# Optimization experiments

Hardware: AMD Instinct MI355X
Metric: run time of the kernel (lower is better)

Reference implementation:

```python
import jax, jax.numpy as jnp
import numpy as np
import math

DROPOUT_P = 0.3

def setup_inputs() -> dict:
    key = jax.random.key(0)
    ks = jax.random.split(key, 8)
    B, S, D, H = 16, 2048, 1024, 128
    x = jax.random.normal(ks[0], (B, S, D), dtype=jnp.float32)
    attention_mask = jax.random.randint(ks[1], (B, S), 0, 2, dtype=jnp.int32)
    qw = 0.02 * jax.random.normal(ks[2], (H, D), dtype=jnp.float32)
    kw = 0.02 * jax.random.normal(ks[3], (H, D), dtype=jnp.float32)
    vw = 0.02 * jax.random.normal(ks[4], (H, D), dtype=jnp.float32)
    qb = jnp.zeros((H,), jnp.float32)
    kb = jnp.zeros((H,), jnp.float32)
    vb = jnp.zeros((H,), jnp.float32)
    return {"x": x, "attention_mask": attention_mask, "qw": qw, "qb": qb,
            "kw": kw, "kb": kb, "vw": vw, "vb": vb}

def reference(x, attention_mask, qw, qb, kw, kb, vw, vb):
    B, S, _ = x.shape
    H = qw.shape[0]
    # torch Linear: x @ W.T + b
    Q = jnp.einsum('bsd,hd->bsh', x, qw) + qb
    K = jnp.einsum('bsd,hd->bsh', x, kw) + kb
    V = jnp.einsum('bsd,hd->bsh', x, vw) + vb
    scores = jnp.einsum('bqh,bkh->bqk', Q, K) / math.sqrt(H)
    mask = attention_mask[:, None, :]  # [B,1,S] broadcast over queries
    scores = jnp.where(mask == 0, -jnp.inf, scores)
    probs = jax.nn.softmax(scores, axis=-1)
    # training-mode dropout with fixed key (deterministic reference)
    keep = jax.random.bernoulli(jax.random.key(42), 1.0 - DROPOUT_P, probs.shape)
    probs = jnp.where(keep, probs / (1.0 - DROPOUT_P), 0.0)
    out = jnp.einsum('bqk,bkh->bqh', probs, V)
    return out
```

## Files before the change

### kernel.cpp

```cpp
#include <hip/hip_runtime.h>
#include <stdint.h>

#define PRNG_VARIANT 2
#define USE_COMPACTION 1
#define USE_ATTN_MFMA 1

#define B_ 16
#define S_ 2048
#define D_ 1024
#define H_ 128
#define SCALE_ 0.08838834764831845f
#define KEEPP_ 0.7f

typedef __attribute__((ext_vector_type(8))) short bf16x8_t;
typedef __attribute__((ext_vector_type(4))) float f32x4_t;

__device__ __forceinline__ void threefry2x32(uint32_t x0, uint32_t x1,
                                             uint32_t& o0, uint32_t& o1) {
  const uint32_t ks0 = 0u, ks1 = 42u, ks2 = 0x1BD11BF0u;
  x0 += ks0; x1 += ks1;
#define TF_R(r) { x0 += x1; x1 = (x1 << (r)) | (x1 >> (32 - (r))); x1 ^= x0; }
  TF_R(13) TF_R(15) TF_R(26) TF_R(6)
  x0 += ks1; x1 += ks2 + 1u;
  TF_R(17) TF_R(29) TF_R(16) TF_R(24)
  x0 += ks2; x1 += ks0 + 2u;
  TF_R(13) TF_R(15) TF_R(26) TF_R(6)
  x0 += ks0; x1 += ks1 + 3u;
  TF_R(17) TF_R(29) TF_R(16) TF_R(24)
  x0 += ks1; x1 += ks2 + 4u;
  TF_R(13) TF_R(15) TF_R(26) TF_R(6)
  x0 += ks2; x1 += ks0 + 5u;
#undef TF_R
  o0 = x0; o1 = x1;
}

__device__ __forceinline__ bool keep_rand(uint32_t n) {
  uint32_t o0, o1, bits;
#if PRNG_VARIANT == 2
  threefry2x32(0u, n, o0, o1);
  bits = o0 ^ o1;
#elif PRNG_VARIANT == 1
  threefry2x32(0u, n, o0, o1);
  bits = o1;
#else
  if (n < (1u << 25)) { threefry2x32(n, n + (1u << 25), o0, o1); bits = o0; }
  else                { threefry2x32(n - (1u << 25), n, o0, o1); bits = o1; }
#endif
  float u = __uint_as_float((bits >> 9) | 0x3F800000u) - 1.0f;
  return u < KEEPP_;
}

__device__ __forceinline__ uint16_t bf16_rne(float f) {
  uint32_t u = __float_as_uint(f);
  return (uint16_t)((u + 0x7FFFu + ((u >> 16) & 1u)) >> 16);
}

__device__ __forceinline__ bf16x8_t ldf(const ushort* base, int off0, int off1) {
  union { uint2 d[2]; bf16x8_t v; } u;
  u.d[0] = *(const uint2*)(base + off0);
  u.d[1] = *(const uint2*)(base + off1);
  return u.v;
}

__global__ __launch_bounds__(64) void mask_scan(
    const int* __restrict__ amask,
    int* __restrict__ kidx, int* __restrict__ ncomp) {
  const int b = blockIdx.x;
  const int lane = threadIdx.x;
  const int* m = amask + b * S_;
  int* outp = kidx + b * S_;
  int base = 0;
  for (int c = 0; c < S_; c += 64) {
    const int mv = m[c + lane];
    const unsigned long long bal = __ballot(mv != 0);
    const int off = __popcll(bal & ((1ull << lane) - 1ull));
    if (mv != 0) outp[base + off] = c + lane;
    base += (int)__popcll(bal);
  }
  if (lane == 0) ncomp[b] = base;
  for (int i = base + lane; i < S_; i += 64) outp[i] = 0;
}

__device__ __forceinline__ bf16x8_t ld_frag(const ushort T[128][36], int row, int g) {
  union { uint2 d[2]; bf16x8_t v; } u;
  u.d[0] = *(const uint2*)&T[row][g << 2];
  u.d[1] = *(const uint2*)&T[row][16 + (g << 2)];
  return u.v;
}

__global__ __launch_bounds__(256) void qkv_mfma(
    const float* __restrict__ x,
    const float* __restrict__ qw, const float* __restrict__ qb,
    const float* __restrict__ kw, const float* __restrict__ kb,
    const float* __restrict__ vw, const float* __restrict__ vb,
    float* __restrict__ qkv) {
  __shared__ ushort Xh[128][36], Xl[128][36], Wh[128][36], Wl[128][36];

  const int tid = threadIdx.x;
  const int m0  = blockIdx.x * 128;
  const int by  = blockIdx.y;
  const float* wsrc = (by == 0) ? qw : (by == 1) ? kw : vw;
  const float* bias = (by == 0) ? qb : (by == 1) ? kb : vb;

  const int wid = tid >> 6, lane = tid & 63;
  const int wy = wid >> 1, wx = wid & 1;
  const int lm = lane & 15, g = lane >> 4;

  const int srow = tid >> 3;
  const int sc4  = (tid & 7) << 2;

  f32x4_t acc[4][4];
#pragma unroll
  for (int i = 0; i < 4; ++i)
#pragma unroll
    for (int j = 0; j < 4; ++j) acc[i][j] = (f32x4_t){0.f, 0.f, 0.f, 0.f};

  for (int k0 = 0; k0 < D_; k0 += 32) {
    __syncthreads();
#pragma unroll
    for (int i = 0; i < 4; ++i) {
      const int row = srow + (i << 5);
      {
        float4 v = *(const float4*)(x + (size_t)(m0 + row) * D_ + k0 + sc4);
        uint16_t h0 = bf16_rne(v.x), h1 = bf16_rne(v.y),
                 h2 = bf16_rne(v.z), h3 = bf16_rne(v.w);
        float r0 = v.x - __uint_as_float((uint32_t)h0 << 16);
        float r1 = v.y - __uint_as_float((uint32_t)h1 << 16);
        float r2 = v.z - __uint_as_float((uint32_t)h2 << 16);
        float r3 = v.w - __uint_as_float((uint32_t)h3 << 16);
        *(uint2*)&Xh[row][sc4] = make_uint2((uint32_t)h0 | ((uint32_t)h1 << 16),
                                            (uint32_t)h2 | ((uint32_t)h3 << 16));
        *(uint2*)&Xl[row][sc4] = make_uint2(
            (uint32_t)bf16_rne(r0) | ((uint32_t)bf16_rne(r1) << 16),
            (uint32_t)bf16_rne(r2) | ((uint32_t)bf16_rne(r3) << 16));
      }
      {
        float4 v = *(const float4*)(wsrc + (size_t)row * D_ + k0 + sc4);
        uint16_t h0 = bf16_rne(v.x), h1 = bf16_rne(v.y),
                 h2 = bf16_rne(v.z), h3 = bf16_rne(v.w);
        float r0 = v.x - __uint_as_float((uint32_t)h0 << 16);
        float r1 = v.y - __uint_as_float((uint32_t)h1 << 16);
        float r2 = v.z - __uint_as_float((uint32_t)h2 << 16);
        float r3 = v.w - __uint_as_float((uint32_t)h3 << 16);
        *(uint2*)&Wh[row][sc4] = make_uint2((uint32_t)h0 | ((uint32_t)h1 << 16),
                                            (uint32_t)h2 | ((uint32_t)h3 << 16));
        *(uint2*)&Wl[row][sc4] = make_uint2(
            (uint32_t)bf16_rne(r0) | ((uint32_t)bf16_rne(r1) << 16),
            (uint32_t)bf16_rne(r2) | ((uint32_t)bf16_rne(r3) << 16));
      }
    }
    __syncthreads();

    bf16x8_t Ah[4], Al[4], Bh[4], Bl[4];
#pragma unroll
    for (int mi = 0; mi < 4; ++mi) {
      const int r = (wy << 6) + (mi << 4) + lm;
      Ah[mi] = ld_frag(Xh, r, g);
      Al[mi] = ld_frag(Xl, r, g);
    }
#pragma unroll
    for (int ni = 0; ni < 4; ++ni) {
      const int r = (wx << 6) + (ni << 4) + lm;
      Bh[ni] = ld_frag(Wh, r, g);
      Bl[ni] = ld_frag(Wl, r, g);
    }
#pragma unroll
    for (int mi = 0; mi < 4; ++mi)
#pragma unroll
      for (int ni = 0; ni < 4; ++ni) {
        acc[mi][ni] = __builtin_amdgcn_mfma_f32_16x16x32_bf16(
            Ah[mi], Bh[ni], acc[mi][ni], 0, 0, 0);
        acc[mi][ni] = __builtin_amdgcn_mfma_f32_16x16x32_bf16(
            Ah[mi], Bl[ni], acc[mi][ni], 0, 0, 0);
        acc[mi][ni] = __builtin_amdgcn_mfma_f32_16x16x32_bf16(
            Al[mi], Bh[ni], acc[mi][ni], 0, 0, 0);
      }
  }

#pragma unroll
  for (int mi = 0; mi < 4; ++mi) {
    const int row = m0 + (wy << 6) + (mi << 4) + (g << 2);
#pragma unroll
    for (int ni = 0; ni < 4; ++ni) {
      const int nl = (wx << 6) + (ni << 4) + lm;
      const float bv = bias[nl];
#pragma unroll
      for (int r = 0; r < 4; ++r)
        qkv[(size_t)(row + r) * 384 + (by << 7) + nl] = acc[mi][ni][r] + bv;
    }
  }
}

__global__ __launch_bounds__(128) void attn_mfma(
    const float* __restrict__ qkv,
    const int* __restrict__ kidx,
    const int* __restrict__ ncomp,
    float* __restrict__ out) {
  __shared__ ushort KhS[32][132], KlS[32][132];
  __shared__ ushort Vt[128][36];
  __shared__ int kidx_s[32];

  const int b   = blockIdx.y;
  const int q0  = blockIdx.x * 32;
  const int tid = threadIdx.x;
  const int wid = tid >> 6, lane = tid & 63;
  const int g = lane >> 4, lm = lane & 15;
  const int nc = ncomp[b];
  const int* kidx_b = kidx + b * S_;
  const int qrow = q0 + wid * 16 + lm;

  bf16x8_t Qh[4], Ql[4];
  {
    const float* qptr = qkv + (size_t)(b * S_ + qrow) * 384;
#pragma unroll
    for (int c = 0; c < 4; ++c) {
      float4 ea = *(const float4*)(qptr + 32 * c + 4 * g);
      float4 eb = *(const float4*)(qptr + 32 * c + 16 + 4 * g);
      float f[8] = {ea.x, ea.y, ea.z, ea.w, eb.x, eb.y, eb.z, eb.w};
      union { ushort u[8]; bf16x8_t v; } hh, ll;
#pragma unroll
      for (int e = 0; e < 8; ++e) {
        float s = f[e] * SCALE_;
        ushort h = bf16_rne(s);
        hh.u[e] = h;
        ll.u[e] = bf16_rne(s - __uint_as_float((uint32_t)h << 16));
      }
      Qh[c] = hh.v; Ql[c] = ll.v;
    }
  }

  f32x4_t acc[8];
#pragma unroll
  for (int t = 0; t < 8; ++t) acc[t] = (f32x4_t){0.f, 0.f, 0.f, 0.f};
  float m_run = -INFINITY, l_run = 0.f;
  const uint32_t nq = (uint32_t)(b * S_ + qrow) << 11;

  for (int kt = 0; kt < nc; kt += 32) {
    __syncthreads();
    if (tid < 32) kidx_s[tid] = kidx_b[kt + tid];
#pragma unroll
    for (int i = 0; i < 8; ++i) {
      int flat = i * 128 + tid;
      int key = flat >> 5, c4 = (flat & 31) << 2;
      int krow = kidx_b[kt + key];
      float4 v = *(const float4*)(qkv + ((size_t)(b * S_ + krow) * 384 + 128) + c4);
      uint16_t h0 = bf16_rne(v.x), h1 = bf16_rne(v.y),
               h2 = bf16_rne(v.z), h3 = bf16_rne(v.w);
      float r0 = v.x - __uint_as_float((uint32_t)h0 << 16);
      float r1 = v.y - __uint_as_float((uint32_t)h1 << 16);
      float r2 = v.z - __uint_as_float((uint32_t)h2 << 16);
      float r3 = v.w - __uint_as_float((uint32_t)h3 << 16);
      *(uint2*)&KhS[key][c4] = make_uint2((uint32_t)h0 | ((uint32_t)h1 << 16),
                                          (uint32_t)h2 | ((uint32_t)h3 << 16));
      *(uint2*)&KlS[key][c4] = make_uint2(
          (uint32_t)bf16_rne(r0) | ((uint32_t)bf16_rne(r1) << 16),
          (uint32_t)bf16_rne(r2) | ((uint32_t)bf16_rne(r3) << 16));
    }
#pragma unroll
    for (int i = 0; i < 8; ++i) {
      int flat = i * 128 + tid;
      int key = flat >> 5, c4 = (flat & 31) << 2;
      int krow = kidx_b[kt + key];
      float4 v = *(const float4*)(qkv + ((size_t)(b * S_ + krow) * 384 + 256) + c4);
      Vt[c4 + 0][key] = bf16_rne(v.x);
      Vt[c4 + 1][key] = bf16_rne(v.y);
      Vt[c4 + 2][key] = bf16_rne(v.z);
      Vt[c4 + 3][key] = bf16_rne(v.w);
    }
    __syncthreads();

    f32x4_t s0 = (f32x4_t){0.f, 0.f, 0.f, 0.f};
    f32x4_t s1 = (f32x4_t){0.f, 0.f, 0.f, 0.f};
#pragma unroll
    for (int c = 0; c < 4; ++c) {
      const int o0 = 32 * c + 4 * g, o1 = 32 * c + 16 + 4 * g;
      bf16x8_t a0h = ldf(&KhS[lm][0], o0, o1);
      bf16x8_t a0l = ldf(&KlS[lm][0], o0, o1);
      bf16x8_t a1h = ldf(&KhS[lm + 16][0], o0, o1);
      bf16x8_t a1l = ldf(&KlS[lm + 16][0], o0, o1);
      s0 = __builtin_amdgcn_mfma_f32_16x16x32_bf16(a0h, Qh[c], s0, 0, 0, 0);
      s0 = __builtin_amdgcn_mfma_f32_16x16x32_bf16(a0l, Qh[c], s0, 0, 0, 0);
      s0 = __builtin_amdgcn_mfma_f32_16x16x32_bf16(a0h, Ql[c], s0, 0, 0, 0);
      s1 = __builtin_amdgcn_mfma_f32_16x16x32_bf16(a1h, Qh[c], s1, 0, 0, 0);
      s1 = __builtin_amdgcn_mfma_f32_16x16x32_bf16(a1l, Qh[c], s1, 0, 0, 0);
      s1 = __builtin_amdgcn_mfma_f32_16x16x32_bf16(a1h, Ql[c], s1, 0, 0, 0);
    }

    float sv0[4], sv1[4];
#pragma unroll
    for (int r = 0; r < 4; ++r) {
      sv0[r] = (kt + 4 * g + r      < nc) ? s0[r] : -INFINITY;
      sv1[r] = (kt + 16 + 4 * g + r < nc) ? s1[r] : -INFINITY;
    }
    float tm = fmaxf(fmaxf(fmaxf(sv0[0], sv0[1]), fmaxf(sv0[2], sv0[3])),
                     fmaxf(fmaxf(sv1[0], sv1[1]), fmaxf(sv1[2], sv1[3])));
    tm = fmaxf(tm, __shfl_xor(tm, 16));
    tm = fmaxf(tm, __shfl_xor(tm, 32));
    float mn = fmaxf(m_run, tm);

    float p0[4], p1[4], ps = 0.f;
#pragma unroll
    for (int r = 0; r < 4; ++r) {
      p0[r] = (sv0[r] == -INFINITY) ? 0.f : __expf(sv0[r] - mn);
      p1[r] = (sv1[r] == -INFINITY) ? 0.f : __expf(sv1[r] - mn);
      ps += p0[r] + p1[r];
    }
    ps += __shfl_xor(ps, 16);
    ps += __shfl_xor(ps, 32);

    float rf = (m_run == mn) ? 1.f : __expf(m_run - mn);
    l_run = l_run * rf + ps;
    m_run = mn;

    float fr0 = __shfl(rf, 4 * g + 0);
    float fr1 = __shfl(rf, 4 * g + 1);
    float fr2 = __shfl(rf, 4 * g + 2);
    float fr3 = __shfl(rf, 4 * g + 3);
#pragma unroll
    for (int t = 0; t < 8; ++t) {
      acc[t][0] *= fr0; acc[t][1] *= fr1; acc[t][2] *= fr2; acc[t][3] *= fr3;
    }

    union { ushort u[8]; bf16x8_t v; } pk;
#pragma unroll
    for (int r = 0; r < 4; ++r) {
      float dv0 = keep_rand(nq + (uint32_t)kidx_s[4 * g + r])      ? p0[r] : 0.f;
      float dv1 = keep_rand(nq + (uint32_t)kidx_s[16 + 4 * g + r]) ? p1[r] : 0.f;
      pk.u[r]     = bf16_rne(dv0);
      pk.u[4 + r] = bf16_rne(dv1);
    }

#pragma unroll
    for (int ht = 0; ht < 8; ++ht) {
      bf16x8_t vf = ldf(&Vt[ht * 16 + lm][0], 4 * g, 16 + 4 * g);
      acc[ht] = __builtin_amdgcn_mfma_f32_16x16x32_bf16(pk.v, vf, acc[ht], 0, 0, 0);
    }
  }

  float iv[4];
#pragma unroll
  for (int r = 0; r < 4; ++r) {
    float lq = __shfl(l_run, 4 * g + r);
    iv[r] = 1.0f / (lq * KEEPP_);
  }
#pragma unroll
  for (int ht = 0; ht < 8; ++ht) {
#pragma unroll
    for (int r = 0; r < 4; ++r) {
      const int q = q0 + wid * 16 + 4 * g + r;
      out[(size_t)(b * S_ + q) * H_ + ht * 16 + lm] = acc[ht][r] * iv[r];
    }
  }
}

#if !USE_ATTN_MFMA
__global__ __launch_bounds__(256) void attn_fwd(
    const float* __restrict__ qkv,
    const int* __restrict__ kidx,
    const int* __restrict__ ncomp,
    float* __restrict__ out) {
  __shared__ float Qs[32][132];
  __shared__ float Ks[32][132];

  const int b   = blockIdx.y;
  const int q0  = blockIdx.x * 32;
  const int tid = threadIdx.x;
  const int ty = tid >> 4, tx = tid & 15;
  const int nc = ncomp[b];
  const int* kidx_b = kidx + b * S_;

  const float* qbase = qkv + (size_t)(b * S_ + q0) * 384;
#pragma unroll
  for (int rep = 0; rep < 4; ++rep) {
    int idx = rep * 256 + tid;
    int r = idx >> 5, c4 = (idx & 31) << 2;
    float4 v = *(const float4*)(qbase + (size_t)r * 384 + c4);
    v.x *= SCALE_; v.y *= SCALE_; v.z *= SCALE_; v.w *= SCALE_;
    *(float4*)&Qs[r][c4] = v;
  }

  const int qr = ty * 2;
  const int hx = tx * 8;

  float acc0[8], acc1[8];
#pragma unroll
  for (int h = 0; h < 8; ++h) { acc0[h] = 0.f; acc1[h] = 0.f; }
  float m0v = -INFINITY, m1v = -INFINITY, l0 = 0.f, l1 = 0.f;

  const uint32_t nq0 = (uint32_t)(b * S_ + q0 + qr) << 11;
  const uint32_t nq1 = nq0 + (1u << 11);

  for (int kt = 0; kt < nc; kt += 32) {
    __syncthreads();
#pragma unroll
    for (int rep = 0; rep < 4; ++rep) {
      int idx = rep * 256 + tid;
      int r = idx >> 5, c4 = (idx & 31) << 2;
      int krow = kidx_b[kt + r];
      *(float4*)&Ks[r][c4] =
          *(const float4*)(qkv + ((size_t)(b * S_ + krow) * 384 + 128) + c4);
    }
    const int j0 = kt + tx, j1 = j0 + 16;
    const int kr0 = kidx_b[j0];
    const int kr1 = kidx_b[j1];
    const bool kill0 = (j0 >= nc), kill1 = (j1 >= nc);
    __syncthreads();

    float s00 = 0.f, s01 = 0.f, s10 = 0.f, s11 = 0.f;
#pragma unroll 8
    for (int d = 0; d < 128; d += 4) {
      float4 qv0 = *(const float4*)&Qs[qr][d];
      float4 qv1 = *(const float4*)&Qs[qr + 1][d];
      float4 kv0 = *(const float4*)&Ks[tx][d];
      float4 kv1 = *(const float4*)&Ks[tx + 16][d];
      s00 += qv0.x * kv0.x + qv0.y * kv0.y + qv0.z * kv0.z + qv0.w * kv0.w;
      s01 += qv0.x * kv1.x + qv0.y * kv1.y + qv0.z * kv1.z + qv0.w * kv1.w;
      s10 += qv1.x * kv0.x + qv1.y * kv0.y + qv1.z * kv0.z + qv1.w * kv0.w;
      s11 += qv1.x * kv1.x + qv1.y * kv1.y + qv1.z * kv1.z + qv1.w * kv1.w;
    }
    if (kill0) { s00 = -INFINITY; s10 = -INFINITY; }
    if (kill1) { s01 = -INFINITY; s11 = -INFINITY; }

    float tm0 = fmaxf(s00, s01);
    float tm1 = fmaxf(s10, s11);
#pragma unroll
    for (int o = 1; o < 16; o <<= 1) {
      tm0 = fmaxf(tm0, __shfl_xor(tm0, o, 16));
      tm1 = fmaxf(tm1, __shfl_xor(tm1, o, 16));
    }
    float mn0 = fmaxf(m0v, tm0);
    float mn1 = fmaxf(m1v, tm1);

    float p00 = (s00 == -INFINITY) ? 0.f : __expf(s00 - mn0);
    float p01 = (s01 == -INFINITY) ? 0.f : __expf(s01 - mn0);
    float p10 = (s10 == -INFINITY) ? 0.f : __expf(s10 - mn1);
    float p11 = (s11 == -INFINITY) ? 0.f : __expf(s11 - mn1);

    float ps0 = p00 + p01, ps1 = p10 + p11;
#pragma unroll
    for (int o = 1; o < 16; o <<= 1) {
      ps0 += __shfl_xor(ps0, o, 16);
      ps1 += __shfl_xor(ps1, o, 16);
    }

    float r0 = (m0v == mn0) ? 1.f : __expf(m0v - mn0);
    float r1 = (m1v == mn1) ? 1.f : __expf(m1v - mn1);
    l0 = l0 * r0 + ps0;
    l1 = l1 * r1 + ps1;
#pragma unroll
    for (int h = 0; h < 8; ++h) { acc0[h] *= r0; acc1[h] *= r1; }
    m0v = mn0; m1v = mn1;

    float d00 = keep_rand(nq0 + (uint32_t)kr0) ? p00 : 0.f;
    float d01 = keep_rand(nq0 + (uint32_t)kr1) ? p01 : 0.f;
    float d10 = keep_rand(nq1 + (uint32_t)kr0) ? p10 : 0.f;
    float d11 = keep_rand(nq1 + (uint32_t)kr1) ? p11 : 0.f;

    const float* vb_ = qkv + ((size_t)b * S_) * 384 + 256 + hx;
#pragma unroll 8
    for (int k = 0; k < 16; ++k) {
      float pa = __shfl(d00, k, 16);
      float pb = __shfl(d10, k, 16);
      int vrow = __shfl(kr0, k, 16);
      const float* vr = vb_ + (size_t)vrow * 384;
      float4 va  = *(const float4*)(vr);
      float4 vb2 = *(const float4*)(vr + 4);
      acc0[0] += pa * va.x;  acc0[1] += pa * va.y;
      acc0[2] += pa * va.z;  acc0[3] += pa * va.w;
      acc0[4] += pa * vb2.x; acc0[5] += pa * vb2.y;
      acc0[6] += pa * vb2.z; acc0[7] += pa * vb2.w;
      acc1[0] += pb * va.x;  acc1[1] += pb * va.y;
      acc1[2] += pb * va.z;  acc1[3] += pb * va.w;
      acc1[4] += pb * vb2.x; acc1[5] += pb * vb2.y;
      acc1[6] += pb * vb2.z; acc1[7] += pb * vb2.w;
    }
#pragma unroll 8
    for (int k = 0; k < 16; ++k) {
      float pa = __shfl(d01, k, 16);
      float pb = __shfl(d11, k, 16);
      int vrow = __shfl(kr1, k, 16);
      const float* vr = vb_ + (size_t)vrow * 384;
      float4 va  = *(const float4*)(vr);
      float4 vb2 = *(const float4*)(vr + 4);
      acc0[0] += pa * va.x;  acc0[1] += pa * va.y;
      acc0[2] += pa * va.z;  acc0[3] += pa * va.w;
      acc0[4] += pa * vb2.x; acc0[5] += pa * vb2.y;
      acc0[6] += pa * vb2.z; acc0[7] += pa * vb2.w;
      acc1[0] += pb * va.x;  acc1[1] += pb * va.y;
      acc1[2] += pb * va.z;  acc1[3] += pb * va.w;
      acc1[4] += pb * vb2.x; acc1[5] += pb * vb2.y;
      acc1[6] += pb * vb2.z; acc1[7] += pb * vb2.w;
    }
  }

  const float inv0 = 1.0f / (l0 * KEEPP_);
  const float inv1 = 1.0f / (l1 * KEEPP_);
  float* o0 = out + (size_t)(b * S_ + q0 + qr) * H_ + hx;
  float* o1 = o0 + H_;
  float4 w0 = make_float4(acc0[0] * inv0, acc0[1] * inv0, acc0[2] * inv0, acc0[3] * inv0);
  float4 w1 = make_float4(acc0[4] * inv0, acc0[5] * inv0, acc0[6] * inv0, acc0[7] * inv0);
  float4 w2 = make_float4(acc1[0] * inv1, acc1[1] * inv1, acc1[2] * inv1, acc1[3] * inv1);
  float4 w3 = make_float4(acc1[4] * inv1, acc1[5] * inv1, acc1[6] * inv1, acc1[7] * inv1);
  *(float4*)(o0)     = w0;
  *(float4*)(o0 + 4) = w1;
  *(float4*)(o1)     = w2;
  *(float4*)(o1 + 4) = w3;
}
#endif

extern "C" void kernel_launch(void* const* d_in, const int* in_sizes, int n_in,
                              void* d_out, int out_size, void* d_ws, size_t ws_size,
                              hipStream_t stream) {
  (void)in_sizes; (void)n_in; (void)out_size; (void)ws_size;
  const float* x  = (const float*)d_in[0];
  const int* am   = (const int*)d_in[1];
  const float* qw = (const float*)d_in[2];
  const float* qb = (const float*)d_in[3];
  const float* kw = (const float*)d_in[4];
  const float* kb = (const float*)d_in[5];
  const float* vw = (const float*)d_in[6];
  const float* vb = (const float*)d_in[7];
  float* out = (float*)d_out;

  float* qkv = (float*)d_ws;
  int* kidx  = (int*)((char*)d_ws + (size_t)B_ * S_ * 384 * 4);
  int* ncomp = kidx + B_ * S_;

  mask_scan<<<B_, 64, 0, stream>>>(am, kidx, ncomp);
  qkv_mfma<<<dim3((B_ * S_) / 128, 3), 256, 0, stream>>>(
      x, qw, qb, kw, kb, vw, vb, qkv);
#if USE_ATTN_MFMA
  attn_mfma<<<dim3(S_ / 32, B_), 128, 0, stream>>>(qkv, kidx, ncomp, out);
#else
  attn_fwd<<<dim3(S_ / 32, B_), 256, 0, stream>>>(qkv, kidx, ncomp, out);
#endif
}
```

Measured before the change: 533.5 us.

## Emit K hi/lo and V as bf16 from the projection kernel to shrink attention loads

The QKV projection epilogue now writes Q in fp32 but K pre-split into bf16 hi/lo halves and V as bf16, each to its own contiguous buffer, instead of a single interleaved fp32 qkv buffer. The attention kernel then copies K tiles straight into shared memory without per-tile conversion and loads half-width V. This removes the repeated fp32-to-bf16 splitting of K and V that every query block performed, and halves the bytes fetched per gathered key row. The V transpose tile padding changes from 36 to 34 columns with a matching 32-bit fragment loader, which may alter shared-memory bank conflicts. Dead fallback code and PRNG variants are also removed.

```diff
diff --git a/kernel.cpp b/kernel.cpp
--- a/kernel.cpp
+++ b/kernel.cpp
@@ -2,8 +2,6 @@
 #include <stdint.h>
 
 #define PRNG_VARIANT 2
-#define USE_COMPACTION 1
-#define USE_ATTN_MFMA 1
 
 #define B_ 16
 #define S_ 2048
@@ -35,17 +33,9 @@
 }
 
 __device__ __forceinline__ bool keep_rand(uint32_t n) {
-  uint32_t o0, o1, bits;
-#if PRNG_VARIANT == 2
+  uint32_t o0, o1;
   threefry2x32(0u, n, o0, o1);
-  bits = o0 ^ o1;
-#elif PRNG_VARIANT == 1
-  threefry2x32(0u, n, o0, o1);
-  bits = o1;
-#else
-  if (n < (1u << 25)) { threefry2x32(n, n + (1u << 25), o0, o1); bits = o0; }
-  else                { threefry2x32(n - (1u << 25), n, o0, o1); bits = o1; }
-#endif
+  uint32_t bits = o0 ^ o1;
   float u = __uint_as_float((bits >> 9) | 0x3F800000u) - 1.0f;
   return u < KEEPP_;
 }
@@ -59,6 +49,15 @@
   union { uint2 d[2]; bf16x8_t v; } u;
   u.d[0] = *(const uint2*)(base + off0);
   u.d[1] = *(const uint2*)(base + off1);
+  return u.v;
+}
+
+__device__ __forceinline__ bf16x8_t ldvf(const ushort* rowp, int g) {
+  union { uint d[4]; bf16x8_t v; } u;
+  u.d[0] = *(const uint*)(rowp + 4 * g);
+  u.d[1] = *(const uint*)(rowp + 4 * g + 2);
+  u.d[2] = *(const uint*)(rowp + 16 + 4 * g);
+  u.d[3] = *(const uint*)(rowp + 16 + 4 * g + 2);
   return u.v;
 }
 
@@ -93,7 +92,8 @@
     const float* __restrict__ qw, const float* __restrict__ qb,
     const float* __restrict__ kw, const float* __restrict__ kb,
     const float* __restrict__ vw, const float* __restrict__ vb,
-    float* __restrict__ qkv) {
+    float* __restrict__ qbuf, ushort* __restrict__ khbuf,
+    ushort* __restrict__ klbuf, ushort* __restrict__ vbuf) {
   __shared__ ushort Xh[128][36], Xl[128][36], Wh[128][36], Wl[128][36];
 
   const int tid = threadIdx.x;
@@ -185,19 +185,33 @@
       const int nl = (wx << 6) + (ni << 4) + lm;
       const float bv = bias[nl];
 #pragma unroll
-      for (int r = 0; r < 4; ++r)
-        qkv[(size_t)(row + r) * 384 + (by << 7) + nl] = acc[mi][ni][r] + bv;
+      for (int r = 0; r < 4; ++r) {
+        const float val = acc[mi][ni][r] + bv;
+        const size_t idx = (size_t)(row + r) * H_ + nl;
+        if (by == 0) {
+          qbuf[idx] = val;
+        } else if (by == 1) {
+          uint16_t h = bf16_rne(val);
+          khbuf[idx] = h;
+          klbuf[idx] = bf16_rne(val - __uint_as_float((uint32_t)h << 16));
+        } else {
+          vbuf[idx] = bf16_rne(val);
+        }
+      }
     }
   }
 }
 
 __global__ __launch_bounds__(128) void attn_mfma(
-    const float* __restrict__ qkv,
+    const float* __restrict__ qbuf,
+    const ushort* __restrict__ khbuf,
+    const ushort* __restrict__ klbuf,
+    const ushort* __restrict__ vbuf,
     const int* __restrict__ kidx,
     const int* __restrict__ ncomp,
     float* __restrict__ out) {
   __shared__ ushort KhS[32][132], KlS[32][132];
-  __shared__ ushort Vt[128][36];
+  __shared__ ushort Vt[128][34];
   __shared__ int kidx_s[32];
 
   const int b   = blockIdx.y;
@@ -209,9 +223,13 @@
   const int* kidx_b = kidx + b * S_;
   const int qrow = q0 + wid * 16 + lm;
 
+  const ushort* khp = khbuf + (size_t)b * S_ * H_;
+  const ushort* klp = klbuf + (size_t)b * S_ * H_;
+  const ushort* vbp = vbuf + (size_t)b * S_ * H_;
+
   bf16x8_t Qh[4], Ql[4];
   {
-    const float* qptr = qkv + (size_t)(b * S_ + qrow) * 384;
+    const float* qptr = qbuf + (size_t)(b * S_ + qrow) * H_;
 #pragma unroll
     for (int c = 0; c < 4; ++c) {
       float4 ea = *(const float4*)(qptr + 32 * c + 4 * g);
@@ -243,29 +261,19 @@
       int flat = i * 128 + tid;
       int key = flat >> 5, c4 = (flat & 31) << 2;
       int krow = kidx_b[kt + key];
-      float4 v = *(const float4*)(qkv + ((size_t)(b * S_ + krow) * 384 + 128) + c4);
-      uint16_t h0 = bf16_rne(v.x), h1 = bf16_rne(v.y),
-               h2 = bf16_rne(v.z), h3 = bf16_rne(v.w);
-      float r0 = v.x - __uint_as_float((uint32_t)h0 << 16);
-      float r1 = v.y - __uint_as_float((uint32_t)h1 << 16);
-      float r2 = v.z - __uint_as_float((uint32_t)h2 << 16);
-      float r3 = v.w - __uint_as_float((uint32_t)h3 << 16);
-      *(uint2*)&KhS[key][c4] = make_uint2((uint32_t)h0 | ((uint32_t)h1 << 16),
-                                          (uint32_t)h2 | ((uint32_t)h3 << 16));
-      *(uint2*)&KlS[key][c4] = make_uint2(
-          (uint32_t)bf16_rne(r0) | ((uint32_t)bf16_rne(r1) << 16),
-          (uint32_t)bf16_rne(r2) | ((uint32_t)bf16_rne(r3) << 16));
+      *(uint2*)&KhS[key][c4] = *(const uint2*)(khp + (size_t)krow * H_ + c4);
+      *(uint2*)&KlS[key][c4] = *(const uint2*)(klp + (size_t)krow * H_ + c4);
     }
 #pragma unroll
     for (int i = 0; i < 8; ++i) {
       int flat = i * 128 + tid;
       int key = flat >> 5, c4 = (flat & 31) << 2;
       int krow = kidx_b[kt + key];
-      float4 v = *(const float4*)(qkv + ((size_t)(b * S_ + krow) * 384 + 256) + c4);
-      Vt[c4 + 0][key] = bf16_rne(v.x);
-      Vt[c4 + 1][key] = bf16_rne(v.y);
-      Vt[c4 + 2][key] = bf16_rne(v.z);
-      Vt[c4 + 3][key] = bf16_rne(v.w);
+      uint2 v = *(const uint2*)(vbp + (size_t)krow * H_ + c4);
+      Vt[c4 + 0][key] = (ushort)(v.x & 0xffffu);
+      Vt[c4 + 1][key] = (ushort)(v.x >> 16);
+      Vt[c4 + 2][key] = (ushort)(v.y & 0xffffu);
+      Vt[c4 + 3][key] = (ushort)(v.y >> 16);
     }
     __syncthreads();
 
@@ -332,7 +340,7 @@
 
 #pragma unroll
     for (int ht = 0; ht < 8; ++ht) {
-      bf16x8_t vf = ldf(&Vt[ht * 16 + lm][0], 4 * g, 16 + 4 * g);
+      bf16x8_t vf = ldvf(&Vt[ht * 16 + lm][0], g);
       acc[ht] = __builtin_amdgcn_mfma_f32_16x16x32_bf16(pk.v, vf, acc[ht], 0, 0, 0);
     }
   }
@@ -352,161 +360,6 @@
     }
   }
 }
-
-#if !USE_ATTN_MFMA
-__global__ __launch_bounds__(256) void attn_fwd(
-    const float* __restrict__ qkv,
-    const int* __restrict__ kidx,
-    const int* __restrict__ ncomp,
-    float* __restrict__ out) {
-  __shared__ float Qs[32][132];
-  __shared__ float Ks[32][132];
-
-  const int b   = blockIdx.y;
-  const int q0  = blockIdx.x * 32;
-  const int tid = threadIdx.x;
-  const int ty = tid >> 4, tx = tid & 15;
-  const int nc = ncomp[b];
-  const int* kidx_b = kidx + b * S_;
-
-  const float* qbase = qkv + (size_t)(b * S_ + q0) * 384;
-#pragma unroll
-  for (int rep = 0; rep < 4; ++rep) {
-    int idx = rep * 256 + tid;
-    int r = idx >> 5, c4 = (idx & 31) << 2;
-    float4 v = *(const float4*)(qbase + (size_t)r * 384 + c4);
-    v.x *= SCALE_; v.y *= SCALE_; v.z *= SCALE_; v.w *= SCALE_;
-    *(float4*)&Qs[r][c4] = v;
-  }
-
-  const int qr = ty * 2;
-  const int hx = tx * 8;
-
-  float acc0[8], acc1[8];
-#pragma unroll
-  for (int h = 0; h < 8; ++h) { acc0[h] = 0.f; acc1[h] = 0.f; }
-  float m0v = -INFINITY, m1v = -INFINITY, l0 = 0.f, l1 = 0.f;
-
-  const uint32_t nq0 = (uint32_t)(b * S_ + q0 + qr) << 11;
-  const uint32_t nq1 = nq0 + (1u << 11);
-
-  for (int kt = 0; kt < nc; kt += 32) {
-    __syncthreads();
-#pragma unroll
-    for (int rep = 0; rep < 4; ++rep) {
-      int idx = rep * 256 + tid;
-      int r = idx >> 5, c4 = (idx & 31) << 2;
-      int krow = kidx_b[kt + r];
-      *(float4*)&Ks[r][c4] =
-          *(const float4*)(qkv + ((size_t)(b * S_ + krow) * 384 + 128) + c4);
-    }
-    const int j0 = kt + tx, j1 = j0 + 16;
-    const int kr0 = kidx_b[j0];
-    const int kr1 = kidx_b[j1];
-    const bool kill0 = (j0 >= nc), kill1 = (j1 >= nc);
-    __syncthreads();
-
-    float s00 = 0.f, s01 = 0.f, s10 = 0.f, s11 = 0.f;
-#pragma unroll 8
-    for (int d = 0; d < 128; d += 4) {
-      float4 qv0 = *(const float4*)&Qs[qr][d];
-      float4 qv1 = *(const float4*)&Qs[qr + 1][d];
-      float4 kv0 = *(const float4*)&Ks[tx][d];
-      float4 kv1 = *(const float4*)&Ks[tx + 16][d];
-      s00 += qv0.x * kv0.x + qv0.y * kv0.y + qv0.z * kv0.z + qv0.w * kv0.w;
-      s01 += qv0.x * kv1.x + qv0.y * kv1.y + qv0.z * kv1.z + qv0.w * kv1.w;
-      s10 += qv1.x * kv0.x + qv1.y * kv0.y + qv1.z * kv0.z + qv1.w * kv0.w;
-      s11 += qv1.x * kv1.x + qv1.y * kv1.y + qv1.z * kv1.z + qv1.w * kv1.w;
-    }
-    if (kill0) { s00 = -INFINITY; s10 = -INFINITY; }
-    if (kill1) { s01 = -INFINITY; s11 = -INFINITY; }
-
-    float tm0 = fmaxf(s00, s01);
-    float tm1 = fmaxf(s10, s11);
-#pragma unroll
-    for (int o = 1; o < 16; o <<= 1) {
-      tm0 = fmaxf(tm0, __shfl_xor(tm0, o, 16));
-      tm1 = fmaxf(tm1, __shfl_xor(tm1, o, 16));
-    }
-    float mn0 = fmaxf(m0v, tm0);
-    float mn1 = fmaxf(m1v, tm1);
-
-    float p00 = (s00 == -INFINITY) ? 0.f : __expf(s00 - mn0);
-    float p01 = (s01 == -INFINITY) ? 0.f : __expf(s01 - mn0);
-    float p10 = (s10 == -INFINITY) ? 0.f : __expf(s10 - mn1);
-    float p11 = (s11 == -INFINITY) ? 0.f : __expf(s11 - mn1);
-
-    float ps0 = p00 + p01, ps1 = p10 + p11;
-#pragma unroll
-    for (int o = 1; o < 16; o <<= 1) {
-      ps0 += __shfl_xor(ps0, o, 16);
-      ps1 += __shfl_xor(ps1, o, 16);
-    }
-
-    float r0 = (m0v == mn0) ? 1.f : __expf(m0v - mn0);
-    float r1 = (m1v == mn1) ? 1.f : __expf(m1v - mn1);
-    l0 = l0 * r0 + ps0;
-    l1 = l1 * r1 + ps1;
-#pragma unroll
-    for (int h = 0; h < 8; ++h) { acc0[h] *= r0; acc1[h] *= r1; }
-    m0v = mn0; m1v = mn1;
-
-    float d00 = keep_rand(nq0 + (uint32_t)kr0) ? p00 : 0.f;
-    float d01 = keep_rand(nq0 + (uint32_t)kr1) ? p01 : 0.f;
-    float d10 = keep_rand(nq1 + (uint32_t)kr0) ? p10 : 0.f;
-    float d11 = keep_rand(nq1 + (uint32_t)kr1) ? p11 : 0.f;
-
-    const float* vb_ = qkv + ((size_t)b * S_) * 384 + 256 + hx;
-#pragma unroll 8
-    for (int k = 0; k < 16; ++k) {
-      float pa = __shfl(d00, k, 16);
-      float pb = __shfl(d10, k, 16);
-      int vrow = __shfl(kr0, k, 16);
-      const float* vr = vb_ + (size_t)vrow * 384;
-      float4 va  = *(const float4*)(vr);
-      float4 vb2 = *(const float4*)(vr + 4);
-      acc0[0] += pa * va.x;  acc0[1] += pa * va.y;
-      acc0[2] += pa * va.z;  acc0[3] += pa * va.w;
-      acc0[4] += pa * vb2.x; acc0[5] += pa * vb2.y;
-      acc0[6] += pa * vb2.z; acc0[7] += pa * vb2.w;
-      acc1[0] += pb * va.x;  acc1[1] += pb * va.y;
-      acc1[2] += pb * va.z;  acc1[3] += pb * va.w;
-      acc1[4] += pb * vb2.x; acc1[5] += pb * vb2.y;
-      acc1[6] += pb * vb2.z; acc1[7] += pb * vb2.w;
-    }
-#pragma unroll 8
-    for (int k = 0; k < 16; ++k) {
-      float pa = __shfl(d01, k, 16);
-      float pb = __shfl(d11, k, 16);
-      int vrow = __shfl(kr1, k, 16);
-      const float* vr = vb_ + (size_t)vrow * 384;
-      float4 va  = *(const float4*)(vr);
-      float4 vb2 = *(const float4*)(vr + 4);
-      acc0[0] += pa * va.x;  acc0[1] += pa * va.y;
-      acc0[2] += pa * va.z;  acc0[3] += pa * va.w;
-      acc0[4] += pa * vb2.x; acc0[5] += pa * vb2.y;
-      acc0[6] += pa * vb2.z; acc0[7] += pa * vb2.w;
-      acc1[0] += pb * va.x;  acc1[1] += pb * va.y;
-      acc1[2] += pb * va.z;  acc1[3] += pb * va.w;
-      acc1[4] += pb * vb2.x; acc1[5] += pb * vb2.y;
-      acc1[6] += pb * vb2.z; acc1[7] += pb * vb2.w;
-    }
-  }
-
-  const float inv0 = 1.0f / (l0 * KEEPP_);
-  const float inv1 = 1.0f / (l1 * KEEPP_);
-  float* o0 = out + (size_t)(b * S_ + q0 + qr) * H_ + hx;
-  float* o1 = o0 + H_;
-  float4 w0 = make_float4(acc0[0] * inv0, acc0[1] * inv0, acc0[2] * inv0, acc0[3] * inv0);
-  float4 w1 = make_float4(acc0[4] * inv0, acc0[5] * inv0, acc0[6] * inv0, acc0[7] * inv0);
-  float4 w2 = make_float4(acc1[0] * inv1, acc1[1] * inv1, acc1[2] * inv1, acc1[3] * inv1);
-  float4 w3 = make_float4(acc1[4] * inv1, acc1[5] * inv1, acc1[6] * inv1, acc1[7] * inv1);
-  *(float4*)(o0)     = w0;
-  *(float4*)(o0 + 4) = w1;
-  *(float4*)(o1)     = w2;
-  *(float4*)(o1 + 4) = w3;
-}
-#endif
 
 extern "C" void kernel_launch(void* const* d_in, const int* in_sizes, int n_in,
                               void* d_out, int out_size, void* d_ws, size_t ws_size,
@@ -522,16 +375,17 @@
   const float* vb = (const float*)d_in[7];
   float* out = (float*)d_out;
 
-  float* qkv = (float*)d_ws;
-  int* kidx  = (int*)((char*)d_ws + (size_t)B_ * S_ * 384 * 4);
-  int* ncomp = kidx + B_ * S_;
+  const size_t NE = (size_t)B_ * S_ * H_;
+  float*  qbuf  = (float*)d_ws;
+  ushort* khbuf = (ushort*)((char*)d_ws + NE * 4);
+  ushort* klbuf = khbuf + NE;
+  ushort* vbuf  = klbuf + NE;
+  int*    kidx  = (int*)(vbuf + NE);
+  int*    ncomp = kidx + B_ * S_;
 
   mask_scan<<<B_, 64, 0, stream>>>(am, kidx, ncomp);
   qkv_mfma<<<dim3((B_ * S_) / 128, 3), 256, 0, stream>>>(
-      x, qw, qb, kw, kb, vw, vb, qkv);
-#if USE_ATTN_MFMA
-  attn_mfma<<<dim3(S_ / 32, B_), 128, 0, stream>>>(qkv, kidx, ncomp, out);
-#else
-  attn_fwd<<<dim3(S_ / 32, B_), 256, 0, stream>>>(qkv, kidx, ncomp, out);
-#endif
-}
+      x, qw, qb, kw, kb, vw, vb, qbuf, khbuf, klbuf, vbuf);
+  attn_mfma<<<dim3(S_ / 32, B_), 128, 0, stream>>>(
+      qbuf, khbuf, klbuf, vbuf, kidx, ncomp, out);
+}
```

New measurement: 667.3 us. 1.25x slower.
